# Optimization experiments

Hardware: AMD Instinct MI355X
Metric: run time of the kernel (lower is better)

Reference implementation:

```python
import jax, jax.numpy as jnp
import numpy as np

L, H, P = 16384, 1024, 512
DT_MIN, DT_MAX = 1e-3, 1e-1


def setup_inputs() -> dict:
    key = jax.random.key(0)
    ks = jax.random.split(key, 9)
    input_sequence = jax.random.normal(ks[0], (L, H), dtype=jnp.float32)
    # HiPPO-like diagonal init: negative real parts, spread imaginary parts
    Lambda_re = -0.5 * jnp.ones((P,), dtype=jnp.float32)
    Lambda_im = jnp.pi * jnp.arange(P, dtype=jnp.float32)
    # B_tilde = Vinv @ B with lecun_normal B -> ~N(0, 1/H) entries
    B_re = jax.random.normal(ks[1], (P, H), dtype=jnp.float32) / np.float32(np.sqrt(H))
    B_im = jax.random.normal(ks[2], (P, H), dtype=jnp.float32) / np.float32(np.sqrt(H))
    # C_tilde = C @ V, lecun_normal scale ~1/sqrt(2P)
    C_re = jax.random.normal(ks[3], (H, P), dtype=jnp.float32) / np.float32(np.sqrt(2 * P))
    C_im = jax.random.normal(ks[4], (H, P), dtype=jnp.float32) / np.float32(np.sqrt(2 * P))
    D = jax.random.normal(ks[5], (H,), dtype=jnp.float32)
    # log_step ~ U[log(dt_min), log(dt_max)], shape (P, 1)
    u01 = jax.random.uniform(ks[6], (P, 1), dtype=jnp.float32)
    log_step = jnp.log(DT_MIN) + u01 * (jnp.log(DT_MAX) - jnp.log(DT_MIN))
    return {
        "input_sequence": input_sequence,
        "Lambda_re": Lambda_re, "Lambda_im": Lambda_im,
        "B_re": B_re, "B_im": B_im,
        "C_re": C_re, "C_im": C_im,
        "D": D, "log_step": log_step,
    }


def _binop(q_i, q_j):
    # diagonal linear recurrence combine: x_j = A_j * x_i + b_j
    A_i, b_i = q_i
    A_j, b_j = q_j
    return (A_j * A_i, A_j * b_i + b_j)


def reference(input_sequence, Lambda_re, Lambda_im, B_re, B_im, C_re, C_im, D, log_step):
    # step_rescale = 1.0, clip_eigs = False, conj_sym = True, zoh discretization
    step = jnp.exp(log_step[:, 0])                      # (P,)
    Lam = Lambda_re + 1j * Lambda_im                    # (P,) complex64
    Lambda_bar = jnp.exp(Lam * step)                    # (P,)
    B_tilde = B_re + 1j * B_im                          # (P, H)
    B_bar = ((Lambda_bar - 1.0) / Lam)[:, None] * B_tilde  # (P, H)

    # bf16-split complex matvec: Bu_t = B_bar @ u_t (u real) for all t at once
    Bre_bf = jnp.real(B_bar).astype(jnp.bfloat16)
    Bim_bf = jnp.imag(B_bar).astype(jnp.bfloat16)
    u_bf = input_sequence.astype(jnp.bfloat16)          # (L, H)
    Bu_re = jnp.einsum('ph,lh->lp', Bre_bf, u_bf).astype(jnp.float32)
    Bu_im = jnp.einsum('ph,lh->lp', Bim_bf, u_bf).astype(jnp.float32)
    Bu = Bu_re + 1j * Bu_im                             # (L, P) complex64

    Lambda_elems = Lambda_bar * jnp.ones((input_sequence.shape[0], Lambda_bar.shape[0]),
                                         dtype=Lambda_bar.dtype)  # (L, P)
    _, xs = jax.lax.associative_scan(_binop, (Lambda_elems, Bu))  # xs: (L, P) complex64

    # bf16-split complex matvec y = C_tilde @ x, keep real part only
    Cre_bf = C_re.astype(jnp.bfloat16)
    Cim_bf = C_im.astype(jnp.bfloat16)
    xre_bf = jnp.real(xs).astype(jnp.bfloat16)
    xim_bf = jnp.imag(xs).astype(jnp.bfloat16)
    rr = jnp.einsum('hp,lp->lh', Cre_bf, xre_bf)
    ii = jnp.einsum('hp,lp->lh', Cim_bf, xim_bf)
    y_real = (rr - ii).astype(jnp.float32)              # (L, H)
    ys = 2.0 * y_real                                   # conj_sym doubling

    # feedthrough
    return ys + D * input_sequence
```

## Files before the change

### kernel.cpp

```cpp
#include <hip/hip_runtime.h>
#include <stdint.h>
#include <stddef.h>

#define L_SEQ 16384
#define H_DIM 1024
#define P_DIM 512
#define N2P   1024
#define CHUNK 64
#define NCH   256

#define NB_U 8192
#define NB_B 256
#define NB_C 512
#define NB_T 2

typedef __bf16 bf16x8 __attribute__((ext_vector_type(8)));
typedef float  f32x4  __attribute__((ext_vector_type(4)));
typedef unsigned short u16x8 __attribute__((ext_vector_type(8)));
typedef unsigned int   u32x4 __attribute__((ext_vector_type(4)));

__device__ __forceinline__ unsigned short f2bf(float x) {
  unsigned int u = __float_as_uint(x);
  u += 0x7FFFu + ((u >> 16) & 1u);
  return (unsigned short)(u >> 16);
}
__device__ __forceinline__ float bf2f(unsigned short x) {
  return __uint_as_float((unsigned int)x << 16);
}

__global__ void k_pack_all(const float* __restrict__ U, unsigned short* __restrict__ Ub,
                           const float* __restrict__ Bre, const float* __restrict__ Bim,
                           unsigned short* __restrict__ Bp,
                           const float* __restrict__ Cre, const float* __restrict__ Cim,
                           unsigned short* __restrict__ Cp,
                           const float* __restrict__ Lre, const float* __restrict__ Lim,
                           const float* __restrict__ lstep,
                           float2* __restrict__ lam, float2* __restrict__ lam32,
                           float2* __restrict__ lamK) {
  int bid = blockIdx.x, tid = threadIdx.x;
  if (bid < NB_U) {
    size_t base = ((size_t)bid * 256 + tid) * 8;
    const float4* s = (const float4*)(U + base);
    float4 v0 = s[0], v1 = s[1];
    u16x8 o;
    o[0] = f2bf(v0.x); o[1] = f2bf(v0.y); o[2] = f2bf(v0.z); o[3] = f2bf(v0.w);
    o[4] = f2bf(v1.x); o[5] = f2bf(v1.y); o[6] = f2bf(v1.z); o[7] = f2bf(v1.w);
    *(u16x8*)(Ub + base) = o;
  } else if (bid < NB_U + NB_B) {
    int base = ((bid - NB_U) * 256 + tid) * 8;
    int p = base >> 10, h = base & 1023;
    float sv, cv;
    float step = expf(lstep[p]);
    float ar = Lre[p] * step, ai = Lim[p] * step;
    float er = expf(ar);
    sincosf(ai, &sv, &cv);
    float lr = er * cv, li = er * sv;
    float nr = lr - 1.0f, ni = li;
    float dr = Lre[p], di = Lim[p];
    float den = dr * dr + di * di;
    float cx = (nr * dr + ni * di) / den;
    float cy = (ni * dr - nr * di) / den;
    const float4* sre = (const float4*)(Bre + base);
    const float4* sim = (const float4*)(Bim + base);
    float4 r0 = sre[0], r1 = sre[1], i0 = sim[0], i1 = sim[1];
    u16x8 ore, oim;
    ore[0] = f2bf(cx * r0.x - cy * i0.x);  oim[0] = f2bf(cx * i0.x + cy * r0.x);
    ore[1] = f2bf(cx * r0.y - cy * i0.y);  oim[1] = f2bf(cx * i0.y + cy * r0.y);
    ore[2] = f2bf(cx * r0.z - cy * i0.z);  oim[2] = f2bf(cx * i0.z + cy * r0.z);
    ore[3] = f2bf(cx * r0.w - cy * i0.w);  oim[3] = f2bf(cx * i0.w + cy * r0.w);
    ore[4] = f2bf(cx * r1.x - cy * i1.x);  oim[4] = f2bf(cx * i1.x + cy * r1.x);
    ore[5] = f2bf(cx * r1.y - cy * i1.y);  oim[5] = f2bf(cx * i1.y + cy * r1.y);
    ore[6] = f2bf(cx * r1.z - cy * i1.z);  oim[6] = f2bf(cx * i1.z + cy * r1.z);
    ore[7] = f2bf(cx * r1.w - cy * i1.w);  oim[7] = f2bf(cx * i1.w + cy * r1.w);
    *(u16x8*)(Bp + (size_t)(2 * p) * H_DIM + h)     = ore;
    *(u16x8*)(Bp + (size_t)(2 * p + 1) * H_DIM + h) = oim;
  } else if (bid < NB_U + NB_B + NB_C) {
    int base = ((bid - NB_U - NB_B) * 256 + tid) * 8;
    int h = base >> 10, j0 = base & 1023;
    int p0 = j0 >> 1;
    float4 cr = *(const float4*)(Cre + (size_t)h * P_DIM + p0);
    float4 ci = *(const float4*)(Cim + (size_t)h * P_DIM + p0);
    u16x8 o;
    o[0] = f2bf(cr.x); o[1] = f2bf(-ci.x);
    o[2] = f2bf(cr.y); o[3] = f2bf(-ci.y);
    o[4] = f2bf(cr.z); o[5] = f2bf(-ci.z);
    o[6] = f2bf(cr.w); o[7] = f2bf(-ci.w);
    *(u16x8*)(Cp + base) = o;
  } else {
    int p = (bid - NB_U - NB_B - NB_C) * 256 + tid;
    if (p < P_DIM) {
      double step = exp((double)lstep[p]);
      double ar = (double)Lre[p] * step, ai = (double)Lim[p] * step;
      double er = exp(ar);
      lam[p] = make_float2((float)(er * cos(ai)), (float)(er * sin(ai)));
      double ha = 32.0 * ai, hr = exp(32.0 * ar);
      lam32[p] = make_float2((float)(hr * cos(ha)), (float)(hr * sin(ha)));
      double ka = (double)CHUNK * ai, kr = exp((double)CHUNK * ar);
      lamK[p] = make_float2((float)(kr * cos(ka)), (float)(kr * sin(ka)));
    }
  }
}

template <int OUT>
__global__ void gemm_bt(const unsigned short* __restrict__ A,
                        const unsigned short* __restrict__ B,
                        void* __restrict__ Cout,
                        const unsigned short* __restrict__ Ub,
                        const float* __restrict__ Dv) {
  const int K = 1024, N = 1024;
  __shared__ unsigned short sA[128 * 64];
  __shared__ unsigned short sB[128 * 64];
  const int tid = threadIdx.x;
  const int wave = tid >> 6, lane = tid & 63;
  const int quad = lane >> 4, l16 = lane & 15;
  const int m0 = blockIdx.x * 128, n0 = blockIdx.y * 128;
  const int wm = (wave & 1) * 64, wn = (wave >> 1) * 64;

  f32x4 acc[4][4] = {};

  for (int kt = 0; kt < K; kt += 64) {
    __syncthreads();
#pragma unroll
    for (int r = 0; r < 4; ++r) {
      int s = r * 256 + tid;
      int row = s >> 3;
      int j8 = (s & 7) ^ (row & 7);
      const unsigned short* ga = A + (size_t)(m0 + row) * K + kt + j8 * 8;
      const unsigned short* gb = B + (size_t)(n0 + row) * K + kt + j8 * 8;
      __builtin_amdgcn_global_load_lds(
          (const __attribute__((address_space(1))) unsigned int*)ga,
          (__attribute__((address_space(3))) unsigned int*)(sA + (r * 256 + wave * 64) * 8),
          16, 0, 0);
      __builtin_amdgcn_global_load_lds(
          (const __attribute__((address_space(1))) unsigned int*)gb,
          (__attribute__((address_space(3))) unsigned int*)(sB + (r * 256 + wave * 64) * 8),
          16, 0, 0);
    }
    __syncthreads();

#pragma unroll
    for (int h = 0; h < 2; ++h) {
      bf16x8 af[4], bfr[4];
#pragma unroll
      for (int i = 0; i < 4; ++i) {
        int ra = wm + i * 16 + l16;
        af[i] = *(const bf16x8*)(sA + ra * 64 + (((h << 2) + quad) ^ (ra & 7)) * 8);
      }
#pragma unroll
      for (int j = 0; j < 4; ++j) {
        int rb = wn + j * 16 + l16;
        bfr[j] = *(const bf16x8*)(sB + rb * 64 + (((h << 2) + quad) ^ (rb & 7)) * 8);
      }
#pragma unroll
      for (int i = 0; i < 4; ++i)
#pragma unroll
        for (int j = 0; j < 4; ++j)
          acc[i][j] = __builtin_amdgcn_mfma_f32_16x16x32_bf16(af[i], bfr[j], acc[i][j], 0, 0, 0);
    }
  }

#pragma unroll
  for (int i = 0; i < 4; ++i) {
#pragma unroll
    for (int j = 0; j < 4; ++j) {
      int col = n0 + wn + j * 16 + l16;
#pragma unroll
      for (int r = 0; r < 4; ++r) {
        int row = m0 + wm + i * 16 + quad * 4 + r;
        size_t o = (size_t)row * N + col;
        float v = acc[i][j][r];
        if (OUT) {
          float u = bf2f(Ub[o]);
          ((float*)Cout)[o] = 2.0f * v + Dv[col] * u;
        } else {
          ((unsigned short*)Cout)[o] = f2bf(v);
        }
      }
    }
  }
}

__global__ __launch_bounds__(256) void k_scanA(const unsigned short* __restrict__ Bu,
                                               const float2* __restrict__ lam,
                                               const float2* __restrict__ lam32,
                                               float2* __restrict__ csum) {
  __shared__ unsigned int tile[CHUNK * 128];
  __shared__ float2 comb[128];
  const int bid = blockIdx.x;
  const int chunk = bid >> 2, quarter = bid & 3;
  const int tid = threadIdx.x, wave = tid >> 6;
  const unsigned int* gbase =
      (const unsigned int*)Bu + (size_t)chunk * (CHUNK * 512) + quarter * 128;
#pragma unroll
  for (int r = 0; r < 8; ++r) {
    int g = r * 256 + tid;
    int row = g >> 5, c16 = g & 31;
    __builtin_amdgcn_global_load_lds(
        (const __attribute__((address_space(1))) unsigned int*)
            (gbase + (size_t)row * 512 + c16 * 4),
        (__attribute__((address_space(3))) unsigned int*)(tile + (r * 256 + wave * 64) * 4),
        16, 0, 0);
  }
  __syncthreads();
  const int c = tid & 127, seg = tid >> 7;
  const int p = quarter * 128 + c;
  const float2 l = lam[p];
  const int t0 = seg * 32;
  float xr = 0.f, xi = 0.f;
#pragma unroll 16
  for (int t = 0; t < 32; ++t) {
    unsigned int v = tile[(t0 + t) * 128 + c];
    float br = bf2f((unsigned short)(v & 0xffffu));
    float bi = bf2f((unsigned short)(v >> 16));
    float nr = fmaf(l.x, xr, fmaf(-l.y, xi, br));
    float ni = fmaf(l.x, xi, fmaf(l.y, xr, bi));
    xr = nr; xi = ni;
  }
  if (seg == 0) comb[c] = make_float2(xr, xi);
  __syncthreads();
  if (seg == 1) {
    float2 a = comb[c];
    float2 w = lam32[p];
    float sr = xr + w.x * a.x - w.y * a.y;
    float si = xi + w.x * a.y + w.y * a.x;
    csum[(size_t)chunk * P_DIM + p] = make_float2(sr, si);
  }
}

__global__ __launch_bounds__(256) void k_carry(float2* __restrict__ csum,
                                               const float2* __restrict__ lamK) {
  const int p = blockIdx.x * 256 + threadIdx.x;
  const float2 lk = lamK[p];
  float cr = 0.f, ci = 0.f;
  float2 s = csum[p];
  csum[p] = make_float2(0.f, 0.f);
  for (int c = 1; c < NCH; ++c) {
    float nr = fmaf(lk.x, cr, fmaf(-lk.y, ci, s.x));
    float ni = fmaf(lk.x, ci, fmaf(lk.y, cr, s.y));
    cr = nr; ci = ni;
    s = csum[(size_t)c * P_DIM + p];
    csum[(size_t)c * P_DIM + p] = make_float2(cr, ci);
  }
}

__global__ __launch_bounds__(256) void k_scanC(const unsigned short* __restrict__ Bu,
                                               const float2* __restrict__ lam,
                                               const float2* __restrict__ csum,
                                               unsigned short* __restrict__ xs) {
  __shared__ unsigned int tile[CHUNK * 256];
  const int bid = blockIdx.x;
  const int chunk = bid >> 1, half = bid & 1;
  const int tid = threadIdx.x, wave = tid >> 6, lane = tid & 63;
  const unsigned int* gbase =
      (const unsigned int*)(Bu + (size_t)chunk * CHUNK * N2P) + half * 256;
#pragma unroll
  for (int r = 0; r < 16; ++r) {
    int row = r * 4 + wave;
    __builtin_amdgcn_global_load_lds(
        (const __attribute__((address_space(1))) unsigned int*)
            (gbase + (size_t)row * (N2P / 2) + lane * 4),
        (__attribute__((address_space(3))) unsigned int*)(tile + row * 256),
        16, 0, 0);
  }
  const int p = half * 256 + tid;
  const float2 l = lam[p];
  const float2 seed = csum[(size_t)chunk * P_DIM + p];
  __syncthreads();
  float xr = seed.x, xi = seed.y;
#pragma unroll 16
  for (int t = 0; t < CHUNK; ++t) {
    unsigned int v = tile[t * 256 + tid];
    float br = bf2f((unsigned short)(v & 0xffffu));
    float bi = bf2f((unsigned short)(v >> 16));
    float nr = fmaf(l.x, xr, fmaf(-l.y, xi, br));
    float ni = fmaf(l.x, xi, fmaf(l.y, xr, bi));
    xr = nr; xi = ni;
    tile[t * 256 + tid] = (unsigned int)f2bf(xr) | ((unsigned int)f2bf(xi) << 16);
  }
  __syncthreads();
  unsigned int* obase = (unsigned int*)(xs + (size_t)chunk * CHUNK * N2P) + half * 256;
#pragma unroll
  for (int r = 0; r < 16; ++r) {
    int row = r * 4 + wave;
    *(u32x4*)(obase + (size_t)row * (N2P / 2) + lane * 4) =
        *(const u32x4*)(tile + row * 256 + lane * 4);
  }
}

extern "C" void kernel_launch(void* const* d_in, const int* in_sizes, int n_in,
                              void* d_out, int out_size, void* d_ws, size_t ws_size,
                              hipStream_t stream) {
  const float* U    = (const float*)d_in[0];
  const float* Lre  = (const float*)d_in[1];
  const float* Lim  = (const float*)d_in[2];
  const float* Bre  = (const float*)d_in[3];
  const float* Bim  = (const float*)d_in[4];
  const float* Cre  = (const float*)d_in[5];
  const float* Cim  = (const float*)d_in[6];
  const float* Dv   = (const float*)d_in[7];
  const float* lstp = (const float*)d_in[8];
  float* out = (float*)d_out;

  size_t off = 0;
  char* ws = (char*)d_ws;
  auto give = [&](size_t bytes) -> void* {
    void* p = ws + off;
    off += (bytes + 255) & ~(size_t)255;
    return p;
  };

  unsigned short* ubf  = (unsigned short*)give((size_t)L_SEQ * H_DIM * 2);
  unsigned short* Bp   = (unsigned short*)give((size_t)N2P * H_DIM * 2);
  unsigned short* Cp   = (unsigned short*)give((size_t)H_DIM * N2P * 2);
  unsigned short* Bu   = (unsigned short*)give((size_t)L_SEQ * N2P * 2);
  float2*         lam  = (float2*)give(P_DIM * sizeof(float2));
  float2*         lam32= (float2*)give(P_DIM * sizeof(float2));
  float2*         lamK = (float2*)give(P_DIM * sizeof(float2));
  float2*         csum = (float2*)give((size_t)NCH * P_DIM * sizeof(float2));
  unsigned short* xs   = Bu;

  k_pack_all<<<NB_U + NB_B + NB_C + NB_T, 256, 0, stream>>>(
      U, ubf, Bre, Bim, Bp, Cre, Cim, Cp, Lre, Lim, lstp, lam, lam32, lamK);

  gemm_bt<0><<<dim3(L_SEQ / 128, N2P / 128), 256, 0, stream>>>(ubf, Bp, Bu, nullptr, nullptr);

  k_scanA<<<NCH * 4, 256, 0, stream>>>(Bu, lam, lam32, csum);
  k_carry<<<2, 256, 0, stream>>>(csum, lamK);
  k_scanC<<<NCH * 2, 256, 0, stream>>>(Bu, lam, csum, xs);

  gemm_bt<1><<<dim3(L_SEQ / 128, N2P / 128), 256, 0, stream>>>(xs, Cp, out, ubf, Dv);
}
```

Baseline: 247.5 us.

## Split scanC chunk into two half-chunk segments seeded from scanA partial sums

scanA now also stores the first-half partial state of each chunk. scanC uses 4 blocks per chunk, each covering 128 channels, and splits the 64-step chunk into two 32-step segments per thread. The second segment is seeded from the carry combined with the stored half-chunk state. This halves the serial recurrence length per thread and doubles the block count, at the cost of an extra workspace buffer plus some extra global reads and writes.

```diff
diff --git a/kernel.cpp b/kernel.cpp
--- a/kernel.cpp
+++ b/kernel.cpp
@@ -183,7 +183,8 @@
 __global__ __launch_bounds__(256) void k_scanA(const unsigned short* __restrict__ Bu,
                                                const float2* __restrict__ lam,
                                                const float2* __restrict__ lam32,
-                                               float2* __restrict__ csum) {
+                                               float2* __restrict__ csum,
+                                               float2* __restrict__ csum32) {
   __shared__ unsigned int tile[CHUNK * 128];
   __shared__ float2 comb[128];
   const int bid = blockIdx.x;
@@ -216,7 +217,10 @@
     float ni = fmaf(l.x, xi, fmaf(l.y, xr, bi));
     xr = nr; xi = ni;
   }
-  if (seg == 0) comb[c] = make_float2(xr, xi);
+  if (seg == 0) {
+    comb[c] = make_float2(xr, xi);
+    csum32[(size_t)chunk * P_DIM + p] = make_float2(xr, xi);
+  }
   __syncthreads();
   if (seg == 1) {
     float2 a = comb[c];
@@ -245,45 +249,58 @@
 
 __global__ __launch_bounds__(256) void k_scanC(const unsigned short* __restrict__ Bu,
                                                const float2* __restrict__ lam,
+                                               const float2* __restrict__ lam32,
                                                const float2* __restrict__ csum,
+                                               const float2* __restrict__ csum32,
                                                unsigned short* __restrict__ xs) {
-  __shared__ unsigned int tile[CHUNK * 256];
+  __shared__ unsigned int tile[CHUNK * 128];
   const int bid = blockIdx.x;
-  const int chunk = bid >> 1, half = bid & 1;
-  const int tid = threadIdx.x, wave = tid >> 6, lane = tid & 63;
+  const int chunk = bid >> 2, quarter = bid & 3;
+  const int tid = threadIdx.x, wave = tid >> 6;
   const unsigned int* gbase =
-      (const unsigned int*)(Bu + (size_t)chunk * CHUNK * N2P) + half * 256;
-#pragma unroll
-  for (int r = 0; r < 16; ++r) {
-    int row = r * 4 + wave;
+      (const unsigned int*)Bu + (size_t)chunk * (CHUNK * 512) + quarter * 128;
+#pragma unroll
+  for (int r = 0; r < 8; ++r) {
+    int g = r * 256 + tid;
+    int row = g >> 5, c16 = g & 31;
     __builtin_amdgcn_global_load_lds(
         (const __attribute__((address_space(1))) unsigned int*)
-            (gbase + (size_t)row * (N2P / 2) + lane * 4),
-        (__attribute__((address_space(3))) unsigned int*)(tile + row * 256),
+            (gbase + (size_t)row * 512 + c16 * 4),
+        (__attribute__((address_space(3))) unsigned int*)(tile + (r * 256 + wave * 64) * 4),
         16, 0, 0);
   }
-  const int p = half * 256 + tid;
+  const int c = tid & 127, seg = tid >> 7;
+  const int p = quarter * 128 + c;
   const float2 l = lam[p];
-  const float2 seed = csum[(size_t)chunk * P_DIM + p];
+  const float2 cy = csum[(size_t)chunk * P_DIM + p];
+  float xr, xi;
+  if (seg == 0) {
+    xr = cy.x; xi = cy.y;
+  } else {
+    float2 w = lam32[p];
+    float2 s32 = csum32[(size_t)chunk * P_DIM + p];
+    xr = fmaf(w.x, cy.x, fmaf(-w.y, cy.y, s32.x));
+    xi = fmaf(w.x, cy.y, fmaf(w.y, cy.x, s32.y));
+  }
   __syncthreads();
-  float xr = seed.x, xi = seed.y;
+  const int t0 = seg * 32;
 #pragma unroll 16
-  for (int t = 0; t < CHUNK; ++t) {
-    unsigned int v = tile[t * 256 + tid];
+  for (int t = 0; t < 32; ++t) {
+    unsigned int v = tile[(t0 + t) * 128 + c];
     float br = bf2f((unsigned short)(v & 0xffffu));
     float bi = bf2f((unsigned short)(v >> 16));
     float nr = fmaf(l.x, xr, fmaf(-l.y, xi, br));
     float ni = fmaf(l.x, xi, fmaf(l.y, xr, bi));
     xr = nr; xi = ni;
-    tile[t * 256 + tid] = (unsigned int)f2bf(xr) | ((unsigned int)f2bf(xi) << 16);
+    tile[(t0 + t) * 128 + c] = (unsigned int)f2bf(xr) | ((unsigned int)f2bf(xi) << 16);
   }
   __syncthreads();
-  unsigned int* obase = (unsigned int*)(xs + (size_t)chunk * CHUNK * N2P) + half * 256;
-#pragma unroll
-  for (int r = 0; r < 16; ++r) {
-    int row = r * 4 + wave;
-    *(u32x4*)(obase + (size_t)row * (N2P / 2) + lane * 4) =
-        *(const u32x4*)(tile + row * 256 + lane * 4);
+  unsigned int* ob = (unsigned int*)xs + (size_t)chunk * (CHUNK * 512) + quarter * 128;
+#pragma unroll
+  for (int r = 0; r < 8; ++r) {
+    int g = r * 256 + tid;
+    int row = g >> 5, c16 = g & 31;
+    *(u32x4*)(ob + (size_t)row * 512 + c16 * 4) = *(const u32x4*)(tile + g * 4);
   }
 }
 
@@ -317,6 +334,7 @@
   float2*         lam32= (float2*)give(P_DIM * sizeof(float2));
   float2*         lamK = (float2*)give(P_DIM * sizeof(float2));
   float2*         csum = (float2*)give((size_t)NCH * P_DIM * sizeof(float2));
+  float2*         csum32 = (float2*)give((size_t)NCH * P_DIM * sizeof(float2));
   unsigned short* xs   = Bu;
 
   k_pack_all<<<NB_U + NB_B + NB_C + NB_T, 256, 0, stream>>>(
@@ -324,9 +342,9 @@
 
   gemm_bt<0><<<dim3(L_SEQ / 128, N2P / 128), 256, 0, stream>>>(ubf, Bp, Bu, nullptr, nullptr);
 
-  k_scanA<<<NCH * 4, 256, 0, stream>>>(Bu, lam, lam32, csum);
+  k_scanA<<<NCH * 4, 256, 0, stream>>>(Bu, lam, lam32, csum, csum32);
   k_carry<<<2, 256, 0, stream>>>(csum, lamK);
-  k_scanC<<<NCH * 2, 256, 0, stream>>>(Bu, lam, csum, xs);
+  k_scanC<<<NCH * 4, 256, 0, stream>>>(Bu, lam, lam32, csum, csum32, xs);
 
   gemm_bt<1><<<dim3(L_SEQ / 128, N2P / 128), 256, 0, stream>>>(xs, Cp, out, ubf, Dv);
 }
```

After: 246.4 us. Within noise of the previous version (-0.5%).
